# Kernel tuning notes

Measured on AMD Instinct MI355X. Metric: run time of the kernel, lower is better.

## Reference

```python
import jax, jax.numpy as jnp
import numpy as np

B, S, D, H, DK, DV = 2, 2048, 1024, 16, 64, 64
NEG_INF = -2.0**32 + 1.0  # matches torch module's self.inf


def setup_inputs() -> dict:
    key = jax.random.key(0)
    ks = jax.random.split(key, 9)
    sc = 0.02
    x = jax.random.normal(ks[0], (B, S, D), jnp.float32)
    Wq = jax.random.normal(ks[1], (D, H * DK), jnp.float32) * sc
    bq = jax.random.normal(ks[2], (H * DK,), jnp.float32) * sc
    Wk = jax.random.normal(ks[3], (D, H * DK), jnp.float32) * sc
    bk = jax.random.normal(ks[4], (H * DK,), jnp.float32) * sc
    Wv = jax.random.normal(ks[5], (D, H * DV), jnp.float32) * sc
    bv = jax.random.normal(ks[6], (H * DV,), jnp.float32) * sc
    Wo = jax.random.normal(ks[7], (H * DV, D), jnp.float32) * sc
    bo = jax.random.normal(ks[8], (D,), jnp.float32) * sc
    return {"x": x, "Wq": Wq, "bq": bq, "Wk": Wk, "bk": bk,
            "Wv": Wv, "bv": bv, "Wo": Wo, "bo": bo}


def reference(x, Wq, bq, Wk, bk, Wv, bv, Wo, bo):
    # stage == 'train' path: causal mask applied.
    b, s, _ = x.shape
    # chunk(heads, dim=-1) + cat(dim=0) in torch == per-head split; equivalent
    # math expressed as [B, S, H, d] with head-batched einsums.
    q = (x @ Wq + bq).reshape(b, s, H, DK)
    k = (x @ Wk + bk).reshape(b, s, H, DK)
    v = (x @ Wv + bv).reshape(b, s, H, DV)
    # NOTE: original module does NOT scale by 1/sqrt(dk) — stay faithful.
    score = jnp.einsum('bqhd,bkhd->bhqk', q, k)  # [B, H, S, S]
    causal = jnp.tril(jnp.ones((s, s), dtype=bool))
    score = jnp.where(causal, score, NEG_INF)
    attn = jax.nn.softmax(score, axis=-1)
    ctx = jnp.einsum('bhqk,bkhd->bqhd', attn, v).reshape(b, s, H * DV)
    return ctx @ Wo + bo
```

## Files before the change

### kernel.cpp

```cpp
#include <hip/hip_runtime.h>
#include <stdint.h>

typedef unsigned short u16;
typedef __bf16 bf16_t;
typedef bf16_t bf16x8 __attribute__((ext_vector_type(8)));
typedef float f32x4 __attribute__((ext_vector_type(4)));

#define SB 2048
#define DMODEL 1024
#define NH 16
#define HD 64

__device__ __forceinline__ u16 f2bf(float f) {
  union { float f; uint32_t u; } v; v.f = f;
  uint32_t u = v.u;
  return (u16)((u + 0x7FFFu + ((u >> 16) & 1u)) >> 16);
}

__device__ __forceinline__ void gload16(const void* g, void* l) {
  __builtin_amdgcn_global_load_lds((const __attribute__((address_space(1))) void*)g,
                                   (__attribute__((address_space(3))) void*)l, 16, 0, 0);
}


__global__ __launch_bounds__(256) void k_cvt_x(const float* __restrict__ x, u16* __restrict__ xb) {
  int i = blockIdx.x * 256 + threadIdx.x;
  float4 v = ((const float4*)x)[i];
  uint2 o;
  o.x = (unsigned)f2bf(v.x) | ((unsigned)f2bf(v.y) << 16);
  o.y = (unsigned)f2bf(v.z) | ((unsigned)f2bf(v.w) << 16);
  ((uint2*)xb)[i] = o;
}

__global__ __launch_bounds__(256) void k_transpose_w(
    const float* __restrict__ W0, const float* __restrict__ W1,
    const float* __restrict__ W2, const float* __restrict__ W3,
    u16* __restrict__ T0, u16* __restrict__ T1,
    u16* __restrict__ T2, u16* __restrict__ T3) {
  __shared__ float tile[32][33];
  int mat = blockIdx.z;
  const float* W = (mat == 0) ? W0 : (mat == 1) ? W1 : (mat == 2) ? W2 : W3;
  u16* T = (mat == 0) ? T0 : (mat == 1) ? T1 : (mat == 2) ? T2 : T3;
  int r0 = blockIdx.y * 32, c0 = blockIdx.x * 32;
  int tx = threadIdx.x & 31, ty = threadIdx.x >> 5;
#pragma unroll
  for (int j = 0; j < 4; ++j)
    tile[ty + j * 8][tx] = W[(size_t)(r0 + ty + j * 8) * DMODEL + c0 + tx];
  __syncthreads();
#pragma unroll
  for (int j = 0; j < 4; ++j)
    T[(size_t)(c0 + ty + j * 8) * DMODEL + r0 + tx] = f2bf(tile[tx][ty + j * 8]);
}


__device__ __forceinline__ void gemm_loop(const u16* __restrict__ A, const u16* __restrict__ Bt,
                                          u16* As, u16* Bs, f32x4 (&acc)[4][4]) {
  const int t = threadIdx.x, w = t >> 6, lane = t & 63;
  const int l15 = lane & 15, grp = lane >> 4;
  const int wr = w >> 1, wc = w & 1;
#pragma unroll
  for (int i = 0; i < 4; ++i)
#pragma unroll
    for (int j = 0; j < 4; ++j) acc[i][j] = (f32x4){0.f, 0.f, 0.f, 0.f};

  for (int ks = 0; ks < 16; ++ks) {
    const int k0 = ks * 64;
#pragma unroll
    for (int j = 0; j < 4; ++j) {
      int glin = (w * 4 + j) * 64 + lane;
      int row = glin >> 3;
      int g = (glin & 7) ^ (row & 7);
      gload16(A + (size_t)row * DMODEL + k0 + g * 8, (char*)As + (size_t)(w * 4 + j) * 1024);
      gload16(Bt + (size_t)row * DMODEL + k0 + g * 8, (char*)Bs + (size_t)(w * 4 + j) * 1024);
    }
    __syncthreads();
#pragma unroll
    for (int kk = 0; kk < 2; ++kk) {
      bf16x8 af[4], bfr[4];
#pragma unroll
      for (int i = 0; i < 4; ++i) {
        int row = wr * 64 + i * 16 + l15;
        int g = (4 * kk + grp) ^ (row & 7);
        af[i] = *(const bf16x8*)((const char*)As + row * 128 + (g << 4));
      }
#pragma unroll
      for (int j = 0; j < 4; ++j) {
        int row = wc * 64 + j * 16 + l15;
        int g = (4 * kk + grp) ^ (row & 7);
        bfr[j] = *(const bf16x8*)((const char*)Bs + row * 128 + (g << 4));
      }
#pragma unroll
      for (int i = 0; i < 4; ++i)
#pragma unroll
        for (int j = 0; j < 4; ++j)
          acc[i][j] = __builtin_amdgcn_mfma_f32_16x16x32_bf16(af[i], bfr[j], acc[i][j], 0, 0, 0);
    }
    __syncthreads();
  }
}


__global__ __launch_bounds__(256) void k_gemm_qk(
    const u16* __restrict__ xb,
    const u16* __restrict__ WqT, const u16* __restrict__ WkT,
    const float* __restrict__ bq, const float* __restrict__ bk,
    u16* __restrict__ Qg, u16* __restrict__ Kg) {
  __shared__ u16 As[128 * 64];
  __shared__ u16 Bs[128 * 64];
  const int nt = blockIdx.x, mt = blockIdx.y;
  const int mat = nt >> 3, n0 = (nt & 7) * 128;
  const u16* Bt = mat ? WkT : WqT;
  const float* bias = mat ? bk : bq;
  u16* out = mat ? Kg : Qg;

  f32x4 acc[4][4];
  gemm_loop(xb + (size_t)mt * 128 * DMODEL, Bt + (size_t)n0 * DMODEL, As, Bs, acc);

  const int t = threadIdx.x, w = t >> 6, lane = t & 63;
  const int l15 = lane & 15, grp = lane >> 4;
  const int wr = w >> 1, wc = w & 1;
#pragma unroll
  for (int i = 0; i < 4; ++i)
#pragma unroll
    for (int j = 0; j < 4; ++j)
#pragma unroll
      for (int r = 0; r < 4; ++r) {
        int mrow = mt * 128 + wr * 64 + i * 16 + 4 * grp + r;
        int ncol = n0 + wc * 64 + j * 16 + l15;
        float v = acc[i][j][r] + bias[ncol];
        int b = mrow >> 11, s2 = mrow & 2047, h = ncol >> 6, d2 = ncol & 63;
        out[((((size_t)b * NH + h) * SB + s2) << 6) + d2] = f2bf(v);
      }
}


__global__ __launch_bounds__(256) void k_gemm_vt(
    const u16* __restrict__ xb, const u16* __restrict__ WvT,
    const float* __restrict__ bv, u16* __restrict__ VTg) {
  __shared__ u16 As[128 * 64];
  __shared__ u16 Bs[128 * 64];
  const int nt = blockIdx.x, mt = blockIdx.y;
  const int n0 = nt * 128;

  f32x4 acc[4][4];
  gemm_loop(WvT + (size_t)mt * 128 * DMODEL, xb + (size_t)n0 * DMODEL, As, Bs, acc);

  const int t = threadIdx.x, w = t >> 6, lane = t & 63;
  const int l15 = lane & 15, grp = lane >> 4;
  const int wr = w >> 1, wc = w & 1;
#pragma unroll
  for (int i = 0; i < 4; ++i)
#pragma unroll
    for (int j = 0; j < 4; ++j)
#pragma unroll
      for (int r = 0; r < 4; ++r) {
        int mrow = mt * 128 + wr * 64 + i * 16 + 4 * grp + r;
        int ncol = n0 + wc * 64 + j * 16 + l15;
        float v = acc[i][j][r] + bv[mrow];
        int b2 = ncol >> 11, key = ncol & 2047, h2 = mrow >> 6, vc = mrow & 63;
        VTg[((((size_t)b2 * NH + h2) << 6) + vc) * SB + key] = f2bf(v);
      }
}


__global__ __launch_bounds__(256) void k_gemm_o(
    const u16* __restrict__ ctx, const u16* __restrict__ WoT,
    const float* __restrict__ bo, float* __restrict__ out) {
  __shared__ u16 As[128 * 64];
  __shared__ u16 Bs[128 * 64];
  const int nt = blockIdx.x, mt = blockIdx.y;

  f32x4 acc[4][4];
  gemm_loop(ctx + (size_t)mt * 128 * DMODEL, WoT + (size_t)nt * 128 * DMODEL, As, Bs, acc);

  const int t = threadIdx.x, w = t >> 6, lane = t & 63;
  const int l15 = lane & 15, grp = lane >> 4;
  const int wr = w >> 1, wc = w & 1;
#pragma unroll
  for (int i = 0; i < 4; ++i)
#pragma unroll
    for (int j = 0; j < 4; ++j)
#pragma unroll
      for (int r = 0; r < 4; ++r) {
        int mrow = mt * 128 + wr * 64 + i * 16 + 4 * grp + r;
        int ncol = nt * 128 + wc * 64 + j * 16 + l15;
        out[(size_t)mrow * DMODEL + ncol] = acc[i][j][r] + bo[ncol];
      }
}


__global__ __launch_bounds__(512) void k_flash(const u16* __restrict__ Qg,
                                               const u16* __restrict__ Kg,
                                               const u16* __restrict__ VTg,
                                               u16* __restrict__ ctx) {
  __shared__ u16 Ks[2][4096];
  __shared__ u16 VTs[2][4096];
  __shared__ u16 Ps[8][1024];
  const int linb = blockIdx.x;
  const int xcd = linb & 7, idx = linb >> 3;
  const int bh = xcd + ((idx & 3) << 3);
  const int pr = idx >> 2;
  const int qt = (pr < 8) ? pr : 23 - pr;
  const int t = threadIdx.x, w = t >> 6, lane = t & 63;
  const int l15 = lane & 15, grp = lane >> 4;
  const size_t bhS = (size_t)bh * SB;
  const u16* Kb = Kg + (bhS << 6);
  const u16* Vb = VTg + (bhS << 6);
  const int b = bh >> 4, h = bh & 15;

  const int qb = qt * 128;
  const int nkt = 2 * qt + 2;
  bf16x8 qf[2];
#pragma unroll
  for (int c = 0; c < 2; ++c)
    qf[c] = *(const bf16x8*)(Qg + ((bhS + qb + w * 16 + l15) << 6) + 32 * c + 8 * grp);
  f32x4 acc[4];
  float plsum[4];
#pragma unroll
  for (int ct = 0; ct < 4; ++ct) acc[ct] = (f32x4){0.f, 0.f, 0.f, 0.f};
#pragma unroll
  for (int j = 0; j < 4; ++j) plsum[j] = 0.f;

  {
    int row = t >> 3, g = (t & 7) ^ (row & 7);
    gload16(Kb + ((size_t)row << 6) + g * 8, (char*)Ks[0] + t * 16);
    gload16(Vb + ((size_t)row << 11) + g * 8, (char*)VTs[0] + t * 16);
  }
  __syncthreads();
  int cur = 0;
  for (int kt = 0; kt < nkt; ++kt) {
    const int kb = kt * 64;
    if (kt + 1 < nkt) {
      int row = t >> 3, g = (t & 7) ^ (row & 7);
      int kb2 = kb + 64;
      gload16(Kb + ((size_t)(kb2 + row) << 6) + g * 8, (char*)Ks[cur ^ 1] + t * 16);
      gload16(Vb + ((size_t)row << 11) + kb2 + g * 8, (char*)VTs[cur ^ 1] + t * 16);
    }
    f32x4 sc[4];
#pragma unroll
    for (int ct = 0; ct < 4; ++ct) {
      sc[ct] = (f32x4){0.f, 0.f, 0.f, 0.f};
#pragma unroll
      for (int c = 0; c < 2; ++c) {
        int row = ct * 16 + l15;
        int g = (4 * c + grp) ^ (row & 7);
        bf16x8 kf = *(const bf16x8*)((const char*)Ks[cur] + row * 128 + (g << 4));
        sc[ct] = __builtin_amdgcn_mfma_f32_16x16x32_bf16(qf[c], kf, sc[ct], 0, 0, 0);
      }
    }
    if (kb + 63 >= qb + w * 16) {
#pragma unroll
      for (int ct = 0; ct < 4; ++ct)
#pragma unroll
        for (int j = 0; j < 4; ++j) {
          int key = kb + ct * 16 + l15, r = qb + w * 16 + 4 * grp + j;
          if (key > r) sc[ct][j] = -1e30f;
        }
    }
#pragma unroll
    for (int ct = 0; ct < 4; ++ct)
#pragma unroll
      for (int j = 0; j < 4; ++j) {
        float p = exp2f(fmaf(sc[ct][j], 1.44269504f, -46.16624130f));
        plsum[j] += p;
        int r = 4 * grp + j, cc = ct * 16 + l15;
        *(u16*)((char*)Ps[w] + r * 128 + (((cc >> 3) ^ (r & 7)) << 4) + (cc & 7) * 2) =
            (u16)(__float_as_uint(p) >> 16);
      }
    asm volatile("s_waitcnt lgkmcnt(0)" ::: "memory");
    __builtin_amdgcn_sched_barrier(0);
#pragma unroll
    for (int ct = 0; ct < 4; ++ct) {
#pragma unroll
      for (int c2 = 0; c2 < 2; ++c2) {
        int pg = (4 * c2 + grp) ^ (l15 & 7);
        bf16x8 pf = *(const bf16x8*)((const char*)Ps[w] + l15 * 128 + (pg << 4));
        int vrow = ct * 16 + l15;
        int vg = (4 * c2 + grp) ^ (vrow & 7);
        bf16x8 vf = *(const bf16x8*)((const char*)VTs[cur] + vrow * 128 + (vg << 4));
        acc[ct] = __builtin_amdgcn_mfma_f32_16x16x32_bf16(pf, vf, acc[ct], 0, 0, 0);
      }
    }
    __syncthreads();
    cur ^= 1;
  }
#pragma unroll
  for (int j = 0; j < 4; ++j) {
#pragma unroll
    for (int d = 1; d < 16; d <<= 1) plsum[j] += __shfl_xor(plsum[j], d, 64);
    float inv = 1.f / plsum[j];
    int rg = qb + w * 16 + 4 * grp + j;
#pragma unroll
    for (int ct = 0; ct < 4; ++ct) {
      int col = h * 64 + ct * 16 + l15;
      ctx[((size_t)b * SB + rg) * DMODEL + col] = f2bf(acc[ct][j] * inv);
    }
  }
}


extern "C" void kernel_launch(void* const* d_in, const int* in_sizes, int n_in,
                              void* d_out, int out_size, void* d_ws, size_t ws_size,
                              hipStream_t stream) {
  const float* x  = (const float*)d_in[0];
  const float* Wq = (const float*)d_in[1];
  const float* bq = (const float*)d_in[2];
  const float* Wk = (const float*)d_in[3];
  const float* bk = (const float*)d_in[4];
  const float* Wv = (const float*)d_in[5];
  const float* bv = (const float*)d_in[6];
  const float* Wo = (const float*)d_in[7];
  const float* bo = (const float*)d_in[8];
  float* out = (float*)d_out;

  char* ws = (char*)d_ws;
  u16* xb  = (u16*)(ws);
  u16* WqT = (u16*)(ws + (8ull  << 20));
  u16* WkT = (u16*)(ws + (10ull << 20));
  u16* WvT = (u16*)(ws + (12ull << 20));
  u16* WoT = (u16*)(ws + (14ull << 20));
  u16* Qg  = (u16*)(ws + (16ull << 20));
  u16* Kg  = (u16*)(ws + (24ull << 20));
  u16* VTg = (u16*)(ws + (32ull << 20));
  u16* ctx = (u16*)(ws + (40ull << 20));

  hipLaunchKernelGGL(k_cvt_x, dim3(4096), dim3(256), 0, stream, x, xb);
  hipLaunchKernelGGL(k_transpose_w, dim3(32, 32, 4), dim3(256), 0, stream,
                     Wq, Wk, Wv, Wo, WqT, WkT, WvT, WoT);
  hipLaunchKernelGGL(k_gemm_qk, dim3(16, 32), dim3(256), 0, stream,
                     xb, WqT, WkT, bq, bk, Qg, Kg);
  hipLaunchKernelGGL(k_gemm_vt, dim3(32, 8), dim3(256), 0, stream, xb, WvT, bv, VTg);
  hipLaunchKernelGGL(k_flash, dim3(512), dim3(512), 0, stream, Qg, Kg, VTg, ctx);
  hipLaunchKernelGGL(k_gemm_o, dim3(8, 32), dim3(256), 0, stream, ctx, WoT, bo, out);
}
```

Baseline: 129.2 us.

## Switch flash attention to 32x32 MFMA with register-resident P and four waves

The attention kernel now uses 32x32x16 bf16 MFMA and computes S transposed (K times Q), so each lane owns one query row. The softmax probabilities are repacked into the PV operand layout through lane shuffles instead of a per-wave LDS round trip, which removes the Ps buffer and its wait. Blocks shrink to 256 threads, with each wave covering 32 query rows and each thread doing two tile loads. The aim is to cut LDS traffic and sync stalls and use larger MFMA tiles, at the cost of more registers per wave and fewer waves per block.

Result: slower. 147.9 us (+14.4%).

```diff
diff --git a/kernel.cpp b/kernel.cpp
--- a/kernel.cpp
+++ b/kernel.cpp
@@ -2,9 +2,11 @@
 #include <stdint.h>
 
 typedef unsigned short u16;
+typedef unsigned int u32;
 typedef __bf16 bf16_t;
 typedef bf16_t bf16x8 __attribute__((ext_vector_type(8)));
 typedef float f32x4 __attribute__((ext_vector_type(4)));
+typedef float f32x16 __attribute__((ext_vector_type(16)));
 
 #define SB 2048
 #define DMODEL 1024
@@ -189,112 +191,122 @@
 }
 
 
-__global__ __launch_bounds__(512) void k_flash(const u16* __restrict__ Qg,
+__global__ __launch_bounds__(256) void k_flash(const u16* __restrict__ Qg,
                                                const u16* __restrict__ Kg,
                                                const u16* __restrict__ VTg,
                                                u16* __restrict__ ctx) {
   __shared__ u16 Ks[2][4096];
   __shared__ u16 VTs[2][4096];
-  __shared__ u16 Ps[8][1024];
   const int linb = blockIdx.x;
   const int xcd = linb & 7, idx = linb >> 3;
   const int bh = xcd + ((idx & 3) << 3);
   const int pr = idx >> 2;
   const int qt = (pr < 8) ? pr : 23 - pr;
   const int t = threadIdx.x, w = t >> 6, lane = t & 63;
-  const int l15 = lane & 15, grp = lane >> 4;
+  const int l31 = lane & 31, hi = lane >> 5;
   const size_t bhS = (size_t)bh * SB;
   const u16* Kb = Kg + (bhS << 6);
   const u16* Vb = VTg + (bhS << 6);
   const int b = bh >> 4, h = bh & 15;
 
   const int qb = qt * 128;
+  const int qw = qb + w * 32;
+  const int myq = qw + l31;
   const int nkt = 2 * qt + 2;
-  bf16x8 qf[2];
-#pragma unroll
-  for (int c = 0; c < 2; ++c)
-    qf[c] = *(const bf16x8*)(Qg + ((bhS + qb + w * 16 + l15) << 6) + 32 * c + 8 * grp);
-  f32x4 acc[4];
-  float plsum[4];
-#pragma unroll
-  for (int ct = 0; ct < 4; ++ct) acc[ct] = (f32x4){0.f, 0.f, 0.f, 0.f};
-#pragma unroll
-  for (int j = 0; j < 4; ++j) plsum[j] = 0.f;
+
+  bf16x8 qf[4];
+#pragma unroll
+  for (int ks = 0; ks < 4; ++ks)
+    qf[ks] = *(const bf16x8*)(Qg + ((bhS + myq) << 6) + ks * 16 + hi * 8);
+
+  f32x16 acc0 = (f32x16)(0.f), acc1 = (f32x16)(0.f);
+  float plsum = 0.f;
 
   {
-    int row = t >> 3, g = (t & 7) ^ (row & 7);
-    gload16(Kb + ((size_t)row << 6) + g * 8, (char*)Ks[0] + t * 16);
-    gload16(Vb + ((size_t)row << 11) + g * 8, (char*)VTs[0] + t * 16);
+#pragma unroll
+    for (int p = 0; p < 2; ++p) {
+      int x = t + p * 256;
+      int row = x >> 3, g = (x & 7) ^ (row & 7);
+      gload16(Kb + ((size_t)row << 6) + g * 8, (char*)Ks[0] + x * 16);
+      gload16(Vb + ((size_t)row << 11) + g * 8, (char*)VTs[0] + x * 16);
+    }
   }
   __syncthreads();
   int cur = 0;
   for (int kt = 0; kt < nkt; ++kt) {
     const int kb = kt * 64;
     if (kt + 1 < nkt) {
-      int row = t >> 3, g = (t & 7) ^ (row & 7);
       int kb2 = kb + 64;
-      gload16(Kb + ((size_t)(kb2 + row) << 6) + g * 8, (char*)Ks[cur ^ 1] + t * 16);
-      gload16(Vb + ((size_t)row << 11) + kb2 + g * 8, (char*)VTs[cur ^ 1] + t * 16);
-    }
-    f32x4 sc[4];
-#pragma unroll
-    for (int ct = 0; ct < 4; ++ct) {
-      sc[ct] = (f32x4){0.f, 0.f, 0.f, 0.f};
-#pragma unroll
-      for (int c = 0; c < 2; ++c) {
-        int row = ct * 16 + l15;
-        int g = (4 * c + grp) ^ (row & 7);
-        bf16x8 kf = *(const bf16x8*)((const char*)Ks[cur] + row * 128 + (g << 4));
-        sc[ct] = __builtin_amdgcn_mfma_f32_16x16x32_bf16(qf[c], kf, sc[ct], 0, 0, 0);
-      }
-    }
-    if (kb + 63 >= qb + w * 16) {
-#pragma unroll
-      for (int ct = 0; ct < 4; ++ct)
-#pragma unroll
-        for (int j = 0; j < 4; ++j) {
-          int key = kb + ct * 16 + l15, r = qb + w * 16 + 4 * grp + j;
-          if (key > r) sc[ct][j] = -1e30f;
+#pragma unroll
+      for (int p = 0; p < 2; ++p) {
+        int x = t + p * 256;
+        int row = x >> 3, g = (x & 7) ^ (row & 7);
+        gload16(Kb + ((size_t)(kb2 + row) << 6) + g * 8, (char*)Ks[cur ^ 1] + x * 16);
+        gload16(Vb + ((size_t)row << 11) + kb2 + g * 8, (char*)VTs[cur ^ 1] + x * 16);
+      }
+    }
+#pragma unroll
+    for (int st = 0; st < 2; ++st) {
+      f32x16 s = (f32x16)(0.f);
+#pragma unroll
+      for (int ks = 0; ks < 4; ++ks) {
+        int row = st * 32 + l31;
+        int byte = (row * 128 + ks * 32 + hi * 16) ^ ((row & 7) << 4);
+        bf16x8 kf = *(const bf16x8*)((const char*)Ks[cur] + byte);
+        s = __builtin_amdgcn_mfma_f32_32x32x16_bf16(kf, qf[ks], s, 0, 0, 0);
+      }
+      if (kb + st * 32 + 31 > qw) {
+#pragma unroll
+        for (int r = 0; r < 16; ++r) {
+          int key = kb + st * 32 + (r & 3) + 8 * (r >> 2) + 4 * hi;
+          if (key > myq) s[r] = -1e30f;
         }
-    }
-#pragma unroll
-    for (int ct = 0; ct < 4; ++ct)
-#pragma unroll
-      for (int j = 0; j < 4; ++j) {
-        float p = exp2f(fmaf(sc[ct][j], 1.44269504f, -46.16624130f));
-        plsum[j] += p;
-        int r = 4 * grp + j, cc = ct * 16 + l15;
-        *(u16*)((char*)Ps[w] + r * 128 + (((cc >> 3) ^ (r & 7)) << 4) + (cc & 7) * 2) =
-            (u16)(__float_as_uint(p) >> 16);
-      }
-    asm volatile("s_waitcnt lgkmcnt(0)" ::: "memory");
-    __builtin_amdgcn_sched_barrier(0);
-#pragma unroll
-    for (int ct = 0; ct < 4; ++ct) {
-#pragma unroll
-      for (int c2 = 0; c2 < 2; ++c2) {
-        int pg = (4 * c2 + grp) ^ (l15 & 7);
-        bf16x8 pf = *(const bf16x8*)((const char*)Ps[w] + l15 * 128 + (pg << 4));
-        int vrow = ct * 16 + l15;
-        int vg = (4 * c2 + grp) ^ (vrow & 7);
-        bf16x8 vf = *(const bf16x8*)((const char*)VTs[cur] + vrow * 128 + (vg << 4));
-        acc[ct] = __builtin_amdgcn_mfma_f32_16x16x32_bf16(pf, vf, acc[ct], 0, 0, 0);
+      }
+      u32 wk[8];
+#pragma unroll
+      for (int i = 0; i < 8; ++i) {
+        float p0 = exp2f(fmaf(s[2 * i], 1.44269504f, -46.16624130f));
+        float p1 = exp2f(fmaf(s[2 * i + 1], 1.44269504f, -46.16624130f));
+        plsum += p0 + p1;
+        wk[i] = (__float_as_uint(p0) >> 16) | (__float_as_uint(p1) & 0xffff0000u);
+      }
+      u32 pw[8];
+#pragma unroll
+      for (int i = 0; i < 8; ++i) pw[i] = __shfl_xor(wk[i], 32, 64);
+      union { u32 u[4]; bf16x8 v; } pa0, pa1;
+      pa0.u[0] = hi ? pw[2] : wk[0];
+      pa0.u[1] = hi ? pw[3] : wk[1];
+      pa0.u[2] = hi ? wk[2] : pw[0];
+      pa0.u[3] = hi ? wk[3] : pw[1];
+      pa1.u[0] = hi ? pw[6] : wk[4];
+      pa1.u[1] = hi ? pw[7] : wk[5];
+      pa1.u[2] = hi ? wk[6] : pw[4];
+      pa1.u[3] = hi ? wk[7] : pw[5];
+#pragma unroll
+      for (int vt = 0; vt < 2; ++vt) {
+#pragma unroll
+        for (int ksl = 0; ksl < 2; ++ksl) {
+          int vrow = vt * 32 + l31;
+          int vbyte = (vrow * 128 + st * 64 + ksl * 32 + hi * 16) ^ ((vrow & 7) << 4);
+          bf16x8 vf = *(const bf16x8*)((const char*)VTs[cur] + vbyte);
+          if (vt == 0)
+            acc0 = __builtin_amdgcn_mfma_f32_32x32x16_bf16(ksl ? pa1.v : pa0.v, vf, acc0, 0, 0, 0);
+          else
+            acc1 = __builtin_amdgcn_mfma_f32_32x32x16_bf16(ksl ? pa1.v : pa0.v, vf, acc1, 0, 0, 0);
+        }
       }
     }
     __syncthreads();
     cur ^= 1;
   }
-#pragma unroll
-  for (int j = 0; j < 4; ++j) {
-#pragma unroll
-    for (int d = 1; d < 16; d <<= 1) plsum[j] += __shfl_xor(plsum[j], d, 64);
-    float inv = 1.f / plsum[j];
-    int rg = qb + w * 16 + 4 * grp + j;
-#pragma unroll
-    for (int ct = 0; ct < 4; ++ct) {
-      int col = h * 64 + ct * 16 + l15;
-      ctx[((size_t)b * SB + rg) * DMODEL + col] = f2bf(acc[ct][j] * inv);
-    }
+  float inv = 1.f / (plsum + __shfl_xor(plsum, 32, 64));
+#pragma unroll
+  for (int r = 0; r < 16; ++r) {
+    int qrow = (r & 3) + 8 * (r >> 2) + 4 * hi;
+    float iv = __shfl(inv, qrow, 64);
+    size_t base = ((size_t)b * SB + qw + qrow) * DMODEL + h * 64 + l31;
+    ctx[base] = f2bf(acc0[r] * iv);
+    ctx[base + 32] = f2bf(acc1[r] * iv);
   }
 }
 
@@ -330,6 +342,6 @@
   hipLaunchKernelGGL(k_gemm_qk, dim3(16, 32), dim3(256), 0, stream,
                      xb, WqT, WkT, bq, bk, Qg, Kg);
   hipLaunchKernelGGL(k_gemm_vt, dim3(32, 8), dim3(256), 0, stream, xb, WvT, bv, VTg);
-  hipLaunchKernelGGL(k_flash, dim3(512), dim3(512), 0, stream, Qg, Kg, VTg, ctx);
+  hipLaunchKernelGGL(k_flash, dim3(512), dim3(256), 0, stream, Qg, Kg, VTg, ctx);
   hipLaunchKernelGGL(k_gemm_o, dim3(8, 32), dim3(256), 0, stream, ctx, WoT, bo, out);
 }
```

## Triple-buffer K/V tiles in flash attention with explicit vmcnt waits

Applied to the files above, without the earlier changes.

Moves the K and V^T shared-memory staging from a double buffer to a triple buffer and prefetches two tiles ahead. The full __syncthreads is replaced by a partial s_waitcnt vmcnt plus s_barrier, so the tile just issued can stay in flight while the next one is consumed. This hides global-load latency better, at the cost of 16 KB more LDS per block, which may reduce occupancy. Correctness depends on the hand-counted vmcnt matching the number of outstanding loads per thread.

After: 129.0 us. Within noise of the previous version (-0.1%).

```diff
diff --git a/kernel.cpp b/kernel.cpp
--- a/kernel.cpp
+++ b/kernel.cpp
@@ -2,6 +2,7 @@
 #include <stdint.h>
 
 typedef unsigned short u16;
+typedef unsigned int u32;
 typedef __bf16 bf16_t;
 typedef bf16_t bf16x8 __attribute__((ext_vector_type(8)));
 typedef float f32x4 __attribute__((ext_vector_type(4)));
@@ -193,8 +194,8 @@
                                                const u16* __restrict__ Kg,
                                                const u16* __restrict__ VTg,
                                                u16* __restrict__ ctx) {
-  __shared__ u16 Ks[2][4096];
-  __shared__ u16 VTs[2][4096];
+  __shared__ u16 Ks[3][4096];
+  __shared__ u16 VTs[3][4096];
   __shared__ u16 Ps[8][1024];
   const int linb = blockIdx.x;
   const int xcd = linb & 7, idx = linb >> 3;
@@ -221,20 +222,25 @@
 #pragma unroll
   for (int j = 0; j < 4; ++j) plsum[j] = 0.f;
 
+  const int srow = t >> 3, sg = ((t & 7) ^ (srow & 7)) * 8;
   {
-    int row = t >> 3, g = (t & 7) ^ (row & 7);
-    gload16(Kb + ((size_t)row << 6) + g * 8, (char*)Ks[0] + t * 16);
-    gload16(Vb + ((size_t)row << 11) + g * 8, (char*)VTs[0] + t * 16);
+    gload16(Kb + ((size_t)srow << 6) + sg, (char*)Ks[0] + t * 16);
+    gload16(Vb + ((size_t)srow << 11) + sg, (char*)VTs[0] + t * 16);
+    gload16(Kb + ((size_t)(64 + srow) << 6) + sg, (char*)Ks[1] + t * 16);
+    gload16(Vb + ((size_t)srow << 11) + 64 + sg, (char*)VTs[1] + t * 16);
   }
-  __syncthreads();
+  asm volatile("s_waitcnt vmcnt(2)" ::: "memory");
+  asm volatile("s_barrier" ::: "memory");
+
   int cur = 0;
   for (int kt = 0; kt < nkt; ++kt) {
     const int kb = kt * 64;
-    if (kt + 1 < nkt) {
-      int row = t >> 3, g = (t & 7) ^ (row & 7);
-      int kb2 = kb + 64;
-      gload16(Kb + ((size_t)(kb2 + row) << 6) + g * 8, (char*)Ks[cur ^ 1] + t * 16);
-      gload16(Vb + ((size_t)row << 11) + kb2 + g * 8, (char*)VTs[cur ^ 1] + t * 16);
+    const bool more = (kt + 2) < nkt;
+    if (more) {
+      int ib = cur ? cur - 1 : 2;
+      int kb2 = kb + 128;
+      gload16(Kb + ((size_t)(kb2 + srow) << 6) + sg, (char*)Ks[ib] + t * 16);
+      gload16(Vb + ((size_t)srow << 11) + kb2 + sg, (char*)VTs[ib] + t * 16);
     }
     f32x4 sc[4];
 #pragma unroll
@@ -281,8 +287,15 @@
         acc[ct] = __builtin_amdgcn_mfma_f32_16x16x32_bf16(pf, vf, acc[ct], 0, 0, 0);
       }
     }
-    __syncthreads();
-    cur ^= 1;
+    if (kt + 1 < nkt) {
+      if (more) {
+        asm volatile("s_waitcnt vmcnt(2)" ::: "memory");
+      } else {
+        asm volatile("s_waitcnt vmcnt(0)" ::: "memory");
+      }
+      asm volatile("s_barrier" ::: "memory");
+    }
+    cur = (cur == 2) ? 0 : cur + 1;
   }
 #pragma unroll
   for (int j = 0; j < 4; ++j) {
```
